# Kernel optimization log

Measured on AMD Instinct MI355X. Metric: run time of the kernel, lower is better.

Reference implementation:

```python
import jax, jax.numpy as jnp
import numpy as np
import math

D_MODEL = 128
NHEAD = 8


def setup_inputs() -> dict:
    key = jax.random.key(0)
    k1, k2 = jax.random.split(key)
    x = jax.random.normal(k1, (1, 128, 64, 64), dtype=jnp.float32)
    # Conv2d(in_c=128, out=3*d_model=384, kernel 1x1, bias=False) -> (384, 128)
    W_qkv = jax.random.normal(k2, (384, 128), dtype=jnp.float32) * (1.0 / math.sqrt(128))
    return {"x": x, "W_qkv": W_qkv}


def reference(x, W_qkv):
    b, c, h, w = x.shape
    n = h * w
    d_head = D_MODEL // NHEAD
    # 1x1 conv == channel-wise linear projection
    qkv = jnp.einsum('bchw,oc->bohw', x, W_qkv)          # (b, 3*d_model, h, w)
    # flatten(2).reshape(b, nhead, -1, h*w).permute(0,1,3,2)
    t = qkv.reshape(b, NHEAD, 3 * d_head, n)
    t = jnp.transpose(t, (0, 1, 3, 2))                   # (b, nhead, n, 3*d_head)
    q, k, v = jnp.split(t, 3, axis=-1)                   # each (b, nhead, n, d_head)
    # NOTE: original scales by sqrt(d_model), not sqrt(d_head)
    scale = 1.0 / math.sqrt(D_MODEL)
    scores = jnp.einsum('bhnd,bhmd->bhnm', q * scale, k)  # (b, nhead, n, n)
    attn = jax.nn.softmax(scores, axis=-1)
    out = jnp.einsum('bhnm,bhmd->bhnd', attn, v)         # (b, nhead, n, d_head)
    out = jnp.transpose(out, (0, 1, 3, 2)).reshape(b, D_MODEL, h, w)
    return out
```

## Files before the change

### kernel.cpp

```cpp
#include <hip/hip_runtime.h>
#include <hip/hip_bf16.h>


typedef __attribute__((ext_vector_type(4))) float    f32x4;
typedef __attribute__((ext_vector_type(8))) short    s16x8;
typedef __attribute__((ext_vector_type(4))) short    s16x4;
typedef __attribute__((ext_vector_type(8))) __bf16   bf16x8;
typedef __attribute__((ext_vector_type(4))) unsigned u32x4;

union FragAB { s16x8 s; bf16x8 b; u32x4 u; };

__device__ __forceinline__ short f2bf(float f) {
    unsigned u = __float_as_uint(f);
    u += 0x7fff + ((u >> 16) & 1);
    return (short)(u >> 16);
}

__device__ __forceinline__ unsigned pkbf(float a, float b) {
    float2 f2; f2.x = a; f2.y = b;
    __hip_bfloat162 h = __float22bfloat162_rn(f2);
    unsigned r;
    __builtin_memcpy(&r, &h, 4);
    return r;
}

#if __has_builtin(__builtin_amdgcn_exp2f)
  #define FASTEXP(x) __builtin_amdgcn_exp2f(x)
  #define QK_SCALE 0.12751744154070513f
#else
  #define FASTEXP(x) __expf(x)
  #define QK_SCALE 0.08838834764831845f
#endif

__global__ __launch_bounds__(256) void qkv_kernel(
    const float* __restrict__ x, const float* __restrict__ w,
    short* __restrict__ qT, short* __restrict__ kv)
{
    __shared__ __align__(16) short xT[4][16][136];
    const int wv   = threadIdx.x >> 6;
    const int lane = threadIdx.x & 63;
    const int colL = lane & 15, quad = lane >> 4;
    const int n0 = blockIdx.x * 64 + wv * 16;
    const int oq = blockIdx.y;

    #pragma unroll
    for (int rr = 0; rr < 4; ++rr) {
        int c  = rr * 32 + (lane >> 1);
        int nh = (lane & 1) * 8;
        f32x4 a = *(const f32x4*)&x[c * 4096 + n0 + nh];
        f32x4 b = *(const f32x4*)&x[c * 4096 + n0 + nh + 4];
        #pragma unroll
        for (int t = 0; t < 4; ++t) {
            xT[wv][nh + t][c]     = f2bf(a[t]);
            xT[wv][nh + 4 + t][c] = f2bf(b[t]);
        }
    }
    __syncthreads();

    FragAB xb[4];
    #pragma unroll
    for (int ks = 0; ks < 4; ++ks)
        xb[ks].s = *(const s16x8*)&xT[wv][colL][ks * 32 + quad * 8];

    const int T    = blockIdx.x;
    const int wloc = wv * 16 + colL;
    const int cc   = wloc >> 5;
    const int bb   = (wloc >> 4) & 1;
    const int qp   = (wloc >> 2) & 3;
    const int jj   = bb * 4 + (wloc & 3);

    #pragma unroll
    for (int i = 0; i < 6; ++i) {
        const int otg  = oq * 6 + i;
        const int ob   = otg * 16;
        const int h    = otg / 3;
        const int kind = otg % 3;
        f32x4 acc = {0.f, 0.f, 0.f, 0.f};
        #pragma unroll
        for (int ks = 0; ks < 4; ++ks) {
            f32x4 wa0 = *(const f32x4*)&w[(ob + colL) * 128 + ks * 32 + quad * 8];
            f32x4 wa1 = *(const f32x4*)&w[(ob + colL) * 128 + ks * 32 + quad * 8 + 4];
            FragAB wa;
            #pragma unroll
            for (int t = 0; t < 4; ++t) {
                wa.s[t]     = f2bf(wa0[t]);
                wa.s[t + 4] = f2bf(wa1[t]);
            }
            acc = __builtin_amdgcn_mfma_f32_16x16x32_bf16(wa.b, xb[ks].b, acc, 0, 0, 0);
        }
        if (kind == 0) {
            s16x4 pk;
            #pragma unroll
            for (int r = 0; r < 4; ++r) pk[r] = f2bf(acc[r] * QK_SCALE);
            *(s16x4*)&qT[(h * 4096 + n0 + colL) * 16 + quad * 4] = pk;
        } else if (kind == 1) {
            s16x4 pk;
            #pragma unroll
            for (int r = 0; r < 4; ++r) pk[r] = f2bf(acc[r]);
            *(s16x4*)&kv[(h * 64 + T) * 2048 + wloc * 16 + quad * 4] = pk;
        } else {
            #pragma unroll
            for (int r = 0; r < 4; ++r) {
                int d = quad * 4 + r;
                kv[(h * 64 + T) * 2048 + 1024 + d * 64 + cc * 32 + qp * 8 + jj] = f2bf(acc[r]);
            }
        }
    }
}

template<int SPLIT>
__global__ __launch_bounds__(256) void attn_kernel(
    const short* __restrict__ qT, const short* __restrict__ kv,
    float* __restrict__ Opart, float* __restrict__ lpart,
    float* __restrict__ out)
{
    const int wv   = threadIdx.x >> 6;
    const int lane = threadIdx.x & 63;
    const int colL = lane & 15, quad = lane >> 4;

    const int bx = blockIdx.x;
    int s, h, b;
    if (SPLIT > 1) { s = bx >> 7; h = (bx >> 4) & 7; b = bx & 15; }
    else           { s = 0;       h = bx >> 4;       b = bx & 15; }
    const int qbase = b * 256 + wv * 64;
    const int nkt = 64 / SPLIT;

    FragAB qfs[4];
    #pragma unroll
    for (int u = 0; u < 4; ++u) {
        qfs[u].s = 0;
        if (quad < 2)
            qfs[u].s = *(const s16x8*)&qT[(h * 4096 + qbase + u * 16 + colL) * 16 + quad * 8];
    }

    FragAB ones;
    #pragma unroll
    for (int j = 0; j < 8; ++j) ones.s[j] = (short)0x3F80;

    f32x4 o[4], ol[4];
    #pragma unroll
    for (int u = 0; u < 4; ++u) {
        o[u]  = (f32x4){0.f, 0.f, 0.f, 0.f};
        ol[u] = (f32x4){0.f, 0.f, 0.f, 0.f};
    }

    const int voffK = colL * 16 + quad * 8;
    const int voffV = 1024 + colL * 64 + quad * 8;

    const short* kvb = kv + (h * 64 + s * nkt) * 2048;

    #pragma unroll
    for (int kt = 0; kt < nkt; ++kt) {
        FragAB kf[4], vf[2];
        #pragma unroll
        for (int t = 0; t < 4; ++t)
            kf[t].s = *(const s16x8*)&kvb[voffK + t * 256];
        #pragma unroll
        for (int c = 0; c < 2; ++c)
            vf[c].s = *(const s16x8*)&kvb[voffV + c * 32];
        kvb += 2048;

        #pragma unroll
        for (int u = 0; u < 4; ++u) {
            f32x4 st[4];
            #pragma unroll
            for (int t = 0; t < 4; ++t) {
                f32x4 z = {0.f, 0.f, 0.f, 0.f};
                st[t] = __builtin_amdgcn_mfma_f32_16x16x32_bf16(kf[t].b, qfs[u].b, z, 0, 0, 0);
            }
            FragAB p0, p1;
            #pragma unroll
            for (int t = 0; t < 2; ++t) {
                p0.u[t * 2 + 0] = pkbf(FASTEXP(st[t][0]), FASTEXP(st[t][1]));
                p0.u[t * 2 + 1] = pkbf(FASTEXP(st[t][2]), FASTEXP(st[t][3]));
                p1.u[t * 2 + 0] = pkbf(FASTEXP(st[t + 2][0]), FASTEXP(st[t + 2][1]));
                p1.u[t * 2 + 1] = pkbf(FASTEXP(st[t + 2][2]), FASTEXP(st[t + 2][3]));
            }
            o[u]  = __builtin_amdgcn_mfma_f32_16x16x32_bf16(vf[0].b, p0.b, o[u],  0, 0, 0);
            ol[u] = __builtin_amdgcn_mfma_f32_16x16x32_bf16(ones.b,  p0.b, ol[u], 0, 0, 0);
            o[u]  = __builtin_amdgcn_mfma_f32_16x16x32_bf16(vf[1].b, p1.b, o[u],  0, 0, 0);
            ol[u] = __builtin_amdgcn_mfma_f32_16x16x32_bf16(ones.b,  p1.b, ol[u], 0, 0, 0);
        }
    }

    #pragma unroll
    for (int u = 0; u < 4; ++u) {
        const float l = ol[u][0];
        const int q0 = qbase + u * 16;
        if (SPLIT > 1) {
            #pragma unroll
            for (int r = 0; r < 4; ++r)
                Opart[((s * 8 + h) * 16 + quad * 4 + r) * 4096 + q0 + colL] = o[u][r];
            if (quad == 0) lpart[(s * 8 + h) * 4096 + q0 + colL] = l;
        } else {
            const float inv = 1.f / l;
            #pragma unroll
            for (int r = 0; r < 4; ++r)
                out[(h * 16 + quad * 4 + r) * 4096 + q0 + colL] = o[u][r] * inv;
        }
    }
}

template<int SPLIT>
__global__ __launch_bounds__(256) void combine_kernel(
    const float* __restrict__ Opart, const float* __restrict__ lpart,
    float* __restrict__ out)
{
    const int row = blockIdx.x >> 2;
    const int n   = (blockIdx.x & 3) * 1024 + threadIdx.x * 4;
    const int h   = row >> 4;
    f32x4 osum = {0.f, 0.f, 0.f, 0.f}, lsum = {0.f, 0.f, 0.f, 0.f};
    #pragma unroll
    for (int s = 0; s < SPLIT; ++s) {
        osum += *(const f32x4*)&Opart[(s * 128 + row) * 4096 + n];
        lsum += *(const f32x4*)&lpart[(s * 8 + h) * 4096 + n];
    }
    f32x4 res;
    #pragma unroll
    for (int r = 0; r < 4; ++r) res[r] = osum[r] / lsum[r];
    *(f32x4*)&out[row * 4096 + n] = res;
}

extern "C" void kernel_launch(void* const* d_in, const int* in_sizes, int n_in,
                              void* d_out, int out_size, void* d_ws, size_t ws_size,
                              hipStream_t stream) {
    const float* x = (const float*)d_in[0];
    const float* w = (const float*)d_in[1];
    float* out = (float*)d_out;

    char* ws = (char*)d_ws;
    short* qT = (short*)ws;
    short* kv = (short*)(ws + (1u << 20));

    constexpr int SPLIT = 8;
    const size_t opart_bytes = (size_t)SPLIT * 128 * 4096 * 4;
    const size_t lpart_bytes = (size_t)SPLIT * 8 * 4096 * 4;
    const size_t need_split  = (3ull << 20) + opart_bytes + lpart_bytes;

    dim3 gq(64, 4);
    qkv_kernel<<<gq, 256, 0, stream>>>(x, w, qT, kv);

    if (ws_size >= need_split) {
        float* Opart = (float*)(ws + (3ull << 20));
        float* lpart = (float*)(ws + (3ull << 20) + opart_bytes);
        attn_kernel<SPLIT><<<SPLIT * 128, 256, 0, stream>>>(qT, kv, Opart, lpart, out);
        combine_kernel<SPLIT><<<512, 256, 0, stream>>>(Opart, lpart, out);
    } else {
        attn_kernel<1><<<128, 256, 0, stream>>>(qT, kv, nullptr, nullptr, out);
    }
}
```

Before: 96.97 us.

## Fuse split-K combine into attention kernel via last-block atomic counter

Removes the separate combine kernel. Each attention block writes its partial O and l, then increments a per-(head, query-block) counter, and the last-arriving split block reduces all partials and writes the normalized output. Counters are zeroed inside the QKV kernel. This saves a kernel launch and its scheduling gap, at the cost of fences, an atomic, and a serialized reduction tail in the final blocks.

Measured after the change: 226.2 us. 2.33x slower.

```diff
diff --git a/kernel.cpp b/kernel.cpp
--- a/kernel.cpp
+++ b/kernel.cpp
@@ -34,7 +34,7 @@
 
 __global__ __launch_bounds__(256) void qkv_kernel(
     const float* __restrict__ x, const float* __restrict__ w,
-    short* __restrict__ qT, short* __restrict__ kv)
+    short* __restrict__ qT, short* __restrict__ kv, int* __restrict__ cnt)
 {
     __shared__ __align__(16) short xT[4][16][136];
     const int wv   = threadIdx.x >> 6;
@@ -43,6 +43,9 @@
     const int n0 = blockIdx.x * 64 + wv * 16;
     const int oq = blockIdx.y;
 
+    if (blockIdx.x == 0 && blockIdx.y == 0 && threadIdx.x < 128)
+        cnt[threadIdx.x] = 0;
+
     #pragma unroll
     for (int rr = 0; rr < 4; ++rr) {
         int c  = rr * 32 + (lane >> 1);
@@ -112,7 +115,7 @@
 __global__ __launch_bounds__(256) void attn_kernel(
     const short* __restrict__ qT, const short* __restrict__ kv,
     float* __restrict__ Opart, float* __restrict__ lpart,
-    float* __restrict__ out)
+    int* __restrict__ cnt, float* __restrict__ out)
 {
     const int wv   = threadIdx.x >> 6;
     const int lane = threadIdx.x & 63;
@@ -183,42 +186,52 @@
         }
     }
 
-    #pragma unroll
-    for (int u = 0; u < 4; ++u) {
-        const float l = ol[u][0];
-        const int q0 = qbase + u * 16;
-        if (SPLIT > 1) {
+    if (SPLIT > 1) {
+        #pragma unroll
+        for (int u = 0; u < 4; ++u) {
+            const int q0 = qbase + u * 16;
             #pragma unroll
             for (int r = 0; r < 4; ++r)
                 Opart[((s * 8 + h) * 16 + quad * 4 + r) * 4096 + q0 + colL] = o[u][r];
-            if (quad == 0) lpart[(s * 8 + h) * 4096 + q0 + colL] = l;
-        } else {
-            const float inv = 1.f / l;
+            if (quad == 0) lpart[(s * 8 + h) * 4096 + q0 + colL] = ol[u][0];
+        }
+
+        __shared__ int isLast;
+        __threadfence();
+        __syncthreads();
+        if (threadIdx.x == 0) {
+            int old = atomicAdd(&cnt[h * 16 + b], 1);
+            isLast = (old == SPLIT - 1);
+        }
+        __syncthreads();
+        if (isLast) {
+            __threadfence();
+            const int q = b * 256 + threadIdx.x;
+            float osum[16];
+            #pragma unroll
+            for (int d = 0; d < 16; ++d) osum[d] = 0.f;
+            float lsum = 0.f;
+            for (int sp = 0; sp < SPLIT; ++sp) {
+                lsum += lpart[(sp * 8 + h) * 4096 + q];
+                #pragma unroll
+                for (int d = 0; d < 16; ++d)
+                    osum[d] += Opart[((sp * 8 + h) * 16 + d) * 4096 + q];
+            }
+            const float inv = 1.f / lsum;
+            #pragma unroll
+            for (int d = 0; d < 16; ++d)
+                out[(h * 16 + d) * 4096 + q] = osum[d] * inv;
+        }
+    } else {
+        #pragma unroll
+        for (int u = 0; u < 4; ++u) {
+            const float inv = 1.f / ol[u][0];
+            const int q0 = qbase + u * 16;
             #pragma unroll
             for (int r = 0; r < 4; ++r)
                 out[(h * 16 + quad * 4 + r) * 4096 + q0 + colL] = o[u][r] * inv;
         }
     }
-}
-
-template<int SPLIT>
-__global__ __launch_bounds__(256) void combine_kernel(
-    const float* __restrict__ Opart, const float* __restrict__ lpart,
-    float* __restrict__ out)
-{
-    const int row = blockIdx.x >> 2;
-    const int n   = (blockIdx.x & 3) * 1024 + threadIdx.x * 4;
-    const int h   = row >> 4;
-    f32x4 osum = {0.f, 0.f, 0.f, 0.f}, lsum = {0.f, 0.f, 0.f, 0.f};
-    #pragma unroll
-    for (int s = 0; s < SPLIT; ++s) {
-        osum += *(const f32x4*)&Opart[(s * 128 + row) * 4096 + n];
-        lsum += *(const f32x4*)&lpart[(s * 8 + h) * 4096 + n];
-    }
-    f32x4 res;
-    #pragma unroll
-    for (int r = 0; r < 4; ++r) res[r] = osum[r] / lsum[r];
-    *(f32x4*)&out[row * 4096 + n] = res;
 }
 
 extern "C" void kernel_launch(void* const* d_in, const int* in_sizes, int n_in,
@@ -235,17 +248,18 @@
     constexpr int SPLIT = 8;
     const size_t opart_bytes = (size_t)SPLIT * 128 * 4096 * 4;
     const size_t lpart_bytes = (size_t)SPLIT * 8 * 4096 * 4;
-    const size_t need_split  = (3ull << 20) + opart_bytes + lpart_bytes;
+    const size_t need_split  = (3ull << 20) + opart_bytes + lpart_bytes + 512;
+
+    float* Opart = (float*)(ws + (3ull << 20));
+    float* lpart = (float*)(ws + (3ull << 20) + opart_bytes);
+    int*   cnt   = (int*)(ws + (3ull << 20) + opart_bytes + lpart_bytes);
 
     dim3 gq(64, 4);
-    qkv_kernel<<<gq, 256, 0, stream>>>(x, w, qT, kv);
+    qkv_kernel<<<gq, 256, 0, stream>>>(x, w, qT, kv, cnt);
 
     if (ws_size >= need_split) {
-        float* Opart = (float*)(ws + (3ull << 20));
-        float* lpart = (float*)(ws + (3ull << 20) + opart_bytes);
-        attn_kernel<SPLIT><<<SPLIT * 128, 256, 0, stream>>>(qT, kv, Opart, lpart, out);
-        combine_kernel<SPLIT><<<512, 256, 0, stream>>>(Opart, lpart, out);
+        attn_kernel<SPLIT><<<SPLIT * 128, 256, 0, stream>>>(qT, kv, Opart, lpart, cnt, out);
     } else {
-        attn_kernel<1><<<128, 256, 0, stream>>>(qT, kv, nullptr, nullptr, out);
-    }
-}
+        attn_kernel<1><<<128, 256, 0, stream>>>(qT, kv, nullptr, nullptr, nullptr, out);
+    }
+}
```
